# Optimization experiments

Measured on AMD Instinct MI355X. Metric: run time of the kernel, lower is better.

The kernel has to match this reference:

```python
import jax, jax.numpy as jnp
import numpy as np

EPS = 1e-8

def setup_inputs() -> dict:
    key = jax.random.key(0)
    k1, k2 = jax.random.split(key)
    B, C, T_text, max_len = 16, 256, 512, 4096
    x = jax.random.normal(k1, (B, C, T_text), dtype=jnp.float32)
    # positive linear-domain durations, mean ~ max_len / T_text = 8
    w = jax.random.uniform(k2, (B, T_text), dtype=jnp.float32) * 16.0
    x_mask = jnp.ones((B, 1, T_text), dtype=jnp.float32)
    y_mask = jnp.ones((B, 1, max_len), dtype=jnp.float32)
    sigma_scale = jnp.ones((1,), dtype=jnp.float32)
    return {"x": x, "w": w, "x_mask": x_mask, "y_mask": y_mask, "sigma_scale": sigma_scale}

def reference(x, w, x_mask, y_mask, sigma_scale):
    # x: (B, C, T_text), w: (B, T_text), y_mask: (B, 1, max_len)
    x = x * x_mask
    center = jnp.cumsum(w, axis=1) - 0.5 * w            # (B, T_text)
    max_len = y_mask.shape[2]
    pos = jnp.arange(max_len, dtype=x.dtype)            # (max_len,)
    mu = pos[None, None, :] - center[:, :, None]        # (B, T_text, max_len)
    sigma = w[:, :, None] * sigma_scale[0]              # (B, T_text, 1)
    weights = jnp.exp(-0.5 * jnp.square(mu) / (jnp.square(sigma) + EPS))
    weights = weights / (jnp.sum(weights, axis=1, keepdims=True) + EPS)
    upsampled = jnp.einsum('bct,btl->bcl', x, weights)  # (B, C, max_len)
    return upsampled * y_mask
```

## Files before the change

### kernel.cpp

```cpp
#include <hip/hip_runtime.h>
#include <hip/hip_bf16.h>

#define EPS 1e-8f

#define BB 16
#define CC 256
#define TT 512
#define LL 4096
#define KC  32
#define TCB 128
#define TLB 32
#define XR  40

typedef __attribute__((ext_vector_type(8))) short short8;
typedef __attribute__((ext_vector_type(4))) float f32x4;

__device__ __forceinline__ unsigned short bfbits(float f) {
    __hip_bfloat16 h = __float2bfloat16(f);
    return *(unsigned short*)&h;
}
__device__ __forceinline__ unsigned int pack2(float lo, float hi) {
    return (unsigned int)bfbits(lo) | ((unsigned int)bfbits(hi) << 16);
}

__global__ __launch_bounds__(512)
void scan_kernel(const float* __restrict__ w,
                 const float* __restrict__ sigma_scale,
                 float* __restrict__ cenG,
                 float* __restrict__ nhG,
                 float* __restrict__ radG) {
    const int b = blockIdx.x;
    const int t = threadIdx.x;
    const int lane = t & 63;
    const int wid  = t >> 6;
    __shared__ float part[8], offs[8];

    const float wv = w[b * TT + t];
    float v = wv;
#pragma unroll
    for (int o = 1; o < 64; o <<= 1) {
        float u = __shfl_up(v, o);
        if (lane >= o) v += u;
    }
    if (lane == 63) part[wid] = v;
    __syncthreads();
    if (t == 0) {
        float run = 0.0f;
#pragma unroll
        for (int i = 0; i < 8; ++i) { offs[i] = run; run += part[i]; }
    }
    __syncthreads();
    const float cum = offs[wid] + v;
    const float ss  = sigma_scale[0];
    const float sg  = wv * ss;
    cenG[b * TT + t] = cum - 0.5f * wv;
    nhG[b * TT + t]  = -0.5f / (sg * sg + EPS);
    radG[b * TT + t] = 6.5f * sg + 1.0f;
}


#define EXPW(tc_, buf_)                                                         \
    {                                                                           \
        const int t0 = (tc_) + tg * 4;                                          \
        const float4 cv = *(const float4*)&cenG[bTT + t0];                      \
        const float4 nv = *(const float4*)&nhG[bTT + t0];                       \
        const float4 xk = *(const float4*)&x_mask[bTT + t0];                    \
        const float posf = (float)(l0 + l_loc);                                 \
        float mu, e0, e1, e2, e3;                                               \
        mu = posf - cv.x; e0 = __expf(mu * mu * nv.x);                          \
        mu = posf - cv.y; e1 = __expf(mu * mu * nv.y);                          \
        mu = posf - cv.z; e2 = __expf(mu * mu * nv.z);                          \
        mu = posf - cv.w; e3 = __expf(mu * mu * nv.w);                          \
        p += (e0 + e1) + (e2 + e3);                                             \
        uint2 pk;                                                               \
        pk.x = pack2(e0 * xk.x, e1 * xk.y);                                     \
        pk.y = pack2(e2 * xk.z, e3 * xk.w);                                     \
        *(uint2*)&ws[buf_][l_loc][tg * 4] = pk;                                 \
    }

#define AFRAG(AF, crow_, tc_)                                                   \
    {                                                                           \
        const float* xp = &x[xbase + (size_t)(crow_) * TT + (tc_) + lg * 8];    \
        const float4 a0 = *(const float4*)xp;                                   \
        const float4 a1 = *(const float4*)(xp + 4);                             \
        uint4 ap;                                                               \
        ap.x = pack2(a0.x, a0.y);                                               \
        ap.y = pack2(a0.z, a0.w);                                               \
        ap.z = pack2(a1.x, a1.y);                                               \
        ap.w = pack2(a1.z, a1.w);                                               \
        AF = *(short8*)&ap;                                                     \
    }

#define MFMA_STEP(buf_, tc_)                                                    \
    {                                                                           \
        short8 af0, af1;                                                        \
        AFRAG(af0, wid * 32 + lq, tc_);                                         \
        AFRAG(af1, wid * 32 + 16 + lq, tc_);                                    \
        _Pragma("unroll")                                                       \
        for (int n = 0; n < 2; ++n) {                                           \
            const short8 bfr = *(const short8*)&ws[buf_][n * 16 + lq][lg * 8];  \
            acc0[n] = __builtin_amdgcn_mfma_f32_16x16x32_bf16(af0, bfr, acc0[n], 0, 0, 0); \
            acc1[n] = __builtin_amdgcn_mfma_f32_16x16x32_bf16(af1, bfr, acc1[n], 0, 0, 0); \
        }                                                                       \
    }

__global__ __launch_bounds__(256, 4)
void fused_kernel(const float* __restrict__ x,
                  const float* __restrict__ x_mask,
                  const float* __restrict__ y_mask,
                  const float* __restrict__ cenG,
                  const float* __restrict__ nhG,
                  const float* __restrict__ radG,
                  float* __restrict__ out) {
    __shared__ unsigned short ws[2][TLB][XR];
    __shared__ float dsum[TLB], sscale[TLB];
    __shared__ int tmin_s, tmax_s;

    const int gid = blockIdx.x;
    const int lid = (gid & 7) * 512 + (gid >> 3);
    const int b   = lid >> 8;
    const int rr  = lid & 255;
    const int l0  = (rr >> 1) * TLB;
    const int c0  = (rr & 1) * TCB;

    const int tid  = threadIdx.x;
    const int lane = tid & 63;
    const int wid  = tid >> 6;
    const int lq   = lane & 15;
    const int lg   = lane >> 4;
    const int l_loc = tid >> 3;
    const int tg    = tid & 7;
    const int bTT  = b * TT;
    const size_t xbase = (size_t)(b * CC + c0) * TT;

    if (tid == 0) { tmin_s = TT; tmax_s = -1; }
    __syncthreads();

    const float l0f = (float)l0;
    const float l1f = l0f + (float)(TLB - 1);
#pragma unroll
    for (int i = 0; i < 2; ++i) {
        const int tt = tid + 256 * i;
        const float cen = cenG[bTT + tt];
        const float rad = radG[bTT + tt];
        if (cen + rad >= l0f && cen - rad <= l1f) {
            atomicMin(&tmin_s, tt);
            atomicMax(&tmax_s, tt);
        }
    }
    __syncthreads();

    int nch = 0, tlo = 0;
    if (tmax_s >= 0) {
        nch = (tmax_s - tmin_s + KC) / KC;
        tlo = tmin_s;
        if (tlo + nch * KC > TT) tlo = TT - nch * KC;
    }

    f32x4 acc0[2], acc1[2];
#pragma unroll
    for (int n = 0; n < 2; ++n) { acc0[n] = (f32x4)0.0f; acc1[n] = (f32x4)0.0f; }
    float p = 0.0f;

    if (nch > 0) {
        EXPW(tlo, 0);
        __syncthreads();
        for (int i = 0; i < nch; ++i) {
            const int cur = i & 1;
            if (i + 1 < nch) EXPW(tlo + (i + 1) * KC, cur ^ 1);
            MFMA_STEP(cur, tlo + i * KC);
            __syncthreads();
        }
    }

    p += __shfl_xor(p, 1);
    p += __shfl_xor(p, 2);
    p += __shfl_xor(p, 4);
    if ((lane & 7) == 0) dsum[wid * 8 + (lane >> 3)] = p;
    __syncthreads();
    if (tid < TLB)
        sscale[tid] = y_mask[b * LL + l0 + tid] / (dsum[tid] + EPS);
    __syncthreads();

    const float sc0 = sscale[lq];
    const float sc1 = sscale[16 + lq];
    const size_t obase = (size_t)(b * CC + c0) * LL + l0;
#pragma unroll
    for (int r = 0; r < 4; ++r) {
        const int rowA = wid * 32 + lg * 4 + r;
        float* opA = &out[obase + (size_t)rowA * LL];
        opA[lq]      = acc0[0][r] * sc0;
        opA[16 + lq] = acc0[1][r] * sc1;
        float* opB = opA + 16 * LL;
        opB[lq]      = acc1[0][r] * sc0;
        opB[16 + lq] = acc1[1][r] * sc1;
    }
}

extern "C" void kernel_launch(void* const* d_in, const int* in_sizes, int n_in,
                              void* d_out, int out_size, void* d_ws, size_t ws_size,
                              hipStream_t stream) {
    const float* x           = (const float*)d_in[0];
    const float* w           = (const float*)d_in[1];
    const float* x_mask      = (const float*)d_in[2];
    const float* y_mask      = (const float*)d_in[3];
    const float* sigma_scale = (const float*)d_in[4];
    float* out = (float*)d_out;

    float* cenG = (float*)d_ws;
    float* nhG  = cenG + BB * TT;
    float* radG = nhG + BB * TT;

    hipLaunchKernelGGL(scan_kernel, dim3(BB), dim3(512), 0, stream,
                       w, sigma_scale, cenG, nhG, radG);
    hipLaunchKernelGGL(fused_kernel,
                       dim3((LL / TLB) * (CC / TCB) * BB), dim3(256), 0, stream,
                       x, x_mask, y_mask, cenG, nhG, radG, out);
}
```

Before: 28.76 us.

## Fuse cumsum scan into main kernel and process four L sub-tiles per block

Removes the separate scan kernel: each block now recomputes the per-batch cumulative sum, centers, and inverse variances into shared memory. To amortize that redundant scan, each block covers 128 output positions as four 32-wide sub-tiles, each with its own T-range window. This saves a kernel launch and global round trips. In exchange it cuts grid size fourfold (1024 blocks), so there is less parallelism, and the sub-tiles are processed serially inside each block.

```diff
diff --git a/kernel.cpp b/kernel.cpp
--- a/kernel.cpp
+++ b/kernel.cpp
@@ -9,7 +9,8 @@
 #define LL 4096
 #define KC  32
 #define TCB 128
-#define TLB 32
+#define TLB 128
+#define SUB 32
 #define XR  40
 
 typedef __attribute__((ext_vector_type(8))) short short8;
@@ -23,49 +24,14 @@
     return (unsigned int)bfbits(lo) | ((unsigned int)bfbits(hi) << 16);
 }
 
-__global__ __launch_bounds__(512)
-void scan_kernel(const float* __restrict__ w,
-                 const float* __restrict__ sigma_scale,
-                 float* __restrict__ cenG,
-                 float* __restrict__ nhG,
-                 float* __restrict__ radG) {
-    const int b = blockIdx.x;
-    const int t = threadIdx.x;
-    const int lane = t & 63;
-    const int wid  = t >> 6;
-    __shared__ float part[8], offs[8];
-
-    const float wv = w[b * TT + t];
-    float v = wv;
-#pragma unroll
-    for (int o = 1; o < 64; o <<= 1) {
-        float u = __shfl_up(v, o);
-        if (lane >= o) v += u;
-    }
-    if (lane == 63) part[wid] = v;
-    __syncthreads();
-    if (t == 0) {
-        float run = 0.0f;
-#pragma unroll
-        for (int i = 0; i < 8; ++i) { offs[i] = run; run += part[i]; }
-    }
-    __syncthreads();
-    const float cum = offs[wid] + v;
-    const float ss  = sigma_scale[0];
-    const float sg  = wv * ss;
-    cenG[b * TT + t] = cum - 0.5f * wv;
-    nhG[b * TT + t]  = -0.5f / (sg * sg + EPS);
-    radG[b * TT + t] = 6.5f * sg + 1.0f;
-}
-
 
 #define EXPW(tc_, buf_)                                                         \
     {                                                                           \
         const int t0 = (tc_) + tg * 4;                                          \
-        const float4 cv = *(const float4*)&cenG[bTT + t0];                      \
-        const float4 nv = *(const float4*)&nhG[bTT + t0];                       \
-        const float4 xk = *(const float4*)&x_mask[bTT + t0];                    \
-        const float posf = (float)(l0 + l_loc);                                 \
+        const float4 cv = *(const float4*)&cen_s[t0];                           \
+        const float4 nv = *(const float4*)&nh_s[t0];                            \
+        const float4 xk = *(const float4*)&xm_s[t0];                            \
+        const float posf = (float)(ls0 + l_loc);                                \
         float mu, e0, e1, e2, e3;                                               \
         mu = posf - cv.x; e0 = __expf(mu * mu * nv.x);                          \
         mu = posf - cv.y; e1 = __expf(mu * mu * nv.y);                          \
@@ -106,20 +72,21 @@
 
 __global__ __launch_bounds__(256, 4)
 void fused_kernel(const float* __restrict__ x,
+                  const float* __restrict__ w,
                   const float* __restrict__ x_mask,
                   const float* __restrict__ y_mask,
-                  const float* __restrict__ cenG,
-                  const float* __restrict__ nhG,
-                  const float* __restrict__ radG,
+                  const float* __restrict__ sigma_scale,
                   float* __restrict__ out) {
-    __shared__ unsigned short ws[2][TLB][XR];
-    __shared__ float dsum[TLB], sscale[TLB];
-    __shared__ int tmin_s, tmax_s;
+    __shared__ unsigned short ws[2][SUB][XR];
+    __shared__ float cen_s[TT], nh_s[TT], xm_s[TT];
+    __shared__ float dsum[SUB], sscale[SUB];
+    __shared__ float part[4], offs[4];
+    __shared__ int tmn[4], tmx[4];
 
     const int gid = blockIdx.x;
-    const int lid = (gid & 7) * 512 + (gid >> 3);
-    const int b   = lid >> 8;
-    const int rr  = lid & 255;
+    const int lid = (gid & 7) * 128 + (gid >> 3);
+    const int b   = lid >> 6;
+    const int rr  = lid & 63;
     const int l0  = (rr >> 1) * TLB;
     const int c0  = (rr & 1) * TCB;
 
@@ -133,67 +100,104 @@
     const int bTT  = b * TT;
     const size_t xbase = (size_t)(b * CC + c0) * TT;
 
-    if (tid == 0) { tmin_s = TT; tmax_s = -1; }
+    if (tid < 4) { tmn[tid] = TT; tmx[tid] = -1; }
+
+    const int t2 = tid * 2;
+    const float2 w2  = *(const float2*)&w[bTT + t2];
+    const float2 xm2 = *(const float2*)&x_mask[bTT + t2];
+    const float ss = sigma_scale[0];
+    const float pairsum = w2.x + w2.y;
+    float v = pairsum;
+#pragma unroll
+    for (int o = 1; o < 64; o <<= 1) {
+        float u = __shfl_up(v, o);
+        if (lane >= o) v += u;
+    }
+    if (lane == 63) part[wid] = v;
     __syncthreads();
-
-    const float l0f = (float)l0;
-    const float l1f = l0f + (float)(TLB - 1);
-#pragma unroll
-    for (int i = 0; i < 2; ++i) {
-        const int tt = tid + 256 * i;
-        const float cen = cenG[bTT + tt];
-        const float rad = radG[bTT + tt];
-        if (cen + rad >= l0f && cen - rad <= l1f) {
-            atomicMin(&tmin_s, tt);
-            atomicMax(&tmax_s, tt);
-        }
+    if (tid == 0) {
+        float run = 0.0f;
+#pragma unroll
+        for (int i = 0; i < 4; ++i) { offs[i] = run; run += part[i]; }
     }
     __syncthreads();
-
-    int nch = 0, tlo = 0;
-    if (tmax_s >= 0) {
-        nch = (tmax_s - tmin_s + KC) / KC;
-        tlo = tmin_s;
-        if (tlo + nch * KC > TT) tlo = TT - nch * KC;
-    }
-
-    f32x4 acc0[2], acc1[2];
-#pragma unroll
-    for (int n = 0; n < 2; ++n) { acc0[n] = (f32x4)0.0f; acc1[n] = (f32x4)0.0f; }
-    float p = 0.0f;
-
-    if (nch > 0) {
-        EXPW(tlo, 0);
+    const float base = offs[wid] + v - pairsum;
+    const float cum1 = base + w2.x;
+    const float cum2 = cum1 + w2.y;
+    const float cenA = cum1 - 0.5f * w2.x;
+    const float cenB = cum2 - 0.5f * w2.y;
+    cen_s[t2]     = cenA;
+    cen_s[t2 + 1] = cenB;
+    const float sgA = w2.x * ss, sgB = w2.y * ss;
+    nh_s[t2]     = -0.5f / (sgA * sgA + EPS);
+    nh_s[t2 + 1] = -0.5f / (sgB * sgB + EPS);
+    xm_s[t2]     = xm2.x;
+    xm_s[t2 + 1] = xm2.y;
+
+    const float radA = 6.5f * sgA + 1.0f;
+    const float radB = 6.5f * sgB + 1.0f;
+#pragma unroll
+    for (int s = 0; s < 4; ++s) {
+        const float w0 = (float)(l0 + s * SUB);
+        const float w1 = w0 + (float)(SUB - 1);
+        if (cenA + radA >= w0 && cenA - radA <= w1) {
+            atomicMin(&tmn[s], t2); atomicMax(&tmx[s], t2);
+        }
+        if (cenB + radB >= w0 && cenB - radB <= w1) {
+            atomicMin(&tmn[s], t2 + 1); atomicMax(&tmx[s], t2 + 1);
+        }
+    }
+    __syncthreads();
+
+    for (int s = 0; s < 4; ++s) {
+        const int ls0 = l0 + s * SUB;
+        int nch = 0, tlo = 0;
+        if (tmx[s] >= 0) {
+            tlo = tmn[s] & ~3;
+            nch = (tmx[s] - tlo + KC) / KC;
+            const int maxlo = TT - nch * KC;
+            if (tlo > maxlo) tlo = maxlo;
+        }
+
+        f32x4 acc0[2], acc1[2];
+#pragma unroll
+        for (int n = 0; n < 2; ++n) { acc0[n] = (f32x4)0.0f; acc1[n] = (f32x4)0.0f; }
+        float p = 0.0f;
+
+        if (nch > 0) {
+            EXPW(tlo, 0);
+            __syncthreads();
+            for (int i = 0; i < nch; ++i) {
+                const int cur = i & 1;
+                if (i + 1 < nch) EXPW(tlo + (i + 1) * KC, cur ^ 1);
+                MFMA_STEP(cur, tlo + i * KC);
+                __syncthreads();
+            }
+        }
+
+        p += __shfl_xor(p, 1);
+        p += __shfl_xor(p, 2);
+        p += __shfl_xor(p, 4);
+        if ((lane & 7) == 0) dsum[wid * 8 + (lane >> 3)] = p;
         __syncthreads();
-        for (int i = 0; i < nch; ++i) {
-            const int cur = i & 1;
-            if (i + 1 < nch) EXPW(tlo + (i + 1) * KC, cur ^ 1);
-            MFMA_STEP(cur, tlo + i * KC);
-            __syncthreads();
-        }
-    }
-
-    p += __shfl_xor(p, 1);
-    p += __shfl_xor(p, 2);
-    p += __shfl_xor(p, 4);
-    if ((lane & 7) == 0) dsum[wid * 8 + (lane >> 3)] = p;
-    __syncthreads();
-    if (tid < TLB)
-        sscale[tid] = y_mask[b * LL + l0 + tid] / (dsum[tid] + EPS);
-    __syncthreads();
-
-    const float sc0 = sscale[lq];
-    const float sc1 = sscale[16 + lq];
-    const size_t obase = (size_t)(b * CC + c0) * LL + l0;
-#pragma unroll
-    for (int r = 0; r < 4; ++r) {
-        const int rowA = wid * 32 + lg * 4 + r;
-        float* opA = &out[obase + (size_t)rowA * LL];
-        opA[lq]      = acc0[0][r] * sc0;
-        opA[16 + lq] = acc0[1][r] * sc1;
-        float* opB = opA + 16 * LL;
-        opB[lq]      = acc1[0][r] * sc0;
-        opB[16 + lq] = acc1[1][r] * sc1;
+        if (tid < SUB)
+            sscale[tid] = y_mask[b * LL + ls0 + tid] / (dsum[tid] + EPS);
+        __syncthreads();
+
+        const float sc0 = sscale[lq];
+        const float sc1 = sscale[16 + lq];
+        const size_t obase = (size_t)(b * CC + c0) * LL + ls0;
+#pragma unroll
+        for (int r = 0; r < 4; ++r) {
+            const int rowA = wid * 32 + lg * 4 + r;
+            float* opA = &out[obase + (size_t)rowA * LL];
+            opA[lq]      = acc0[0][r] * sc0;
+            opA[16 + lq] = acc0[1][r] * sc1;
+            float* opB = opA + 16 * LL;
+            opB[lq]      = acc1[0][r] * sc0;
+            opB[16 + lq] = acc1[1][r] * sc1;
+        }
+        __syncthreads();
     }
 }
 
@@ -207,13 +211,6 @@
     const float* sigma_scale = (const float*)d_in[4];
     float* out = (float*)d_out;
 
-    float* cenG = (float*)d_ws;
-    float* nhG  = cenG + BB * TT;
-    float* radG = nhG + BB * TT;
-
-    hipLaunchKernelGGL(scan_kernel, dim3(BB), dim3(512), 0, stream,
-                       w, sigma_scale, cenG, nhG, radG);
-    hipLaunchKernelGGL(fused_kernel,
-                       dim3((LL / TLB) * (CC / TCB) * BB), dim3(256), 0, stream,
-                       x, x_mask, y_mask, cenG, nhG, radG, out);
-}
+    hipLaunchKernelGGL(fused_kernel, dim3((LL / TLB) * (CC / TCB) * BB), dim3(256), 0, stream,
+                       x, w, x_mask, y_mask, sigma_scale, out);
+}
```

Measured after the change: 26.44 us. 8.1% less time.
